# Kernel tuning notes

Measured on AMD Instinct MI355X. Metric: run time of the kernel, lower is better.

The kernel has to match this reference:

```python
import jax, jax.numpy as jnp
import numpy as np

N = 100000   # nodes
E = 1600000  # edges
D = 128      # in_channels
H = 128      # hidden_dim
L = 3        # num_layers
LH = 128     # lstm_hidden
OUT = 16     # output_dim
G = 128      # graphs in batch
EPS = 1e-5   # BatchNorm eps


def setup_inputs() -> dict:
    key = jax.random.key(0)
    ks = jax.random.split(key, 14)
    x = jax.random.normal(ks[0], (N, D), jnp.float32)
    src = jax.random.randint(ks[1], (E,), 0, N)
    dst = jax.random.randint(ks[2], (E,), 0, N)
    edge_index = jnp.stack([src, dst])
    batch = jnp.sort(jax.random.randint(ks[3], (N,), 0, G))
    Ws = jax.random.normal(ks[4], (L, D, H), jnp.float32) / np.float32(np.sqrt(D))
    bs = jax.random.normal(ks[5], (L, H), jnp.float32) * 0.02
    gammas = 1.0 + 0.1 * jax.random.normal(ks[6], (L, H), jnp.float32)
    betas = 0.1 * jax.random.normal(ks[7], (L, H), jnp.float32)
    rms = 0.1 * jax.random.normal(ks[8], (L, H), jnp.float32)
    rvs = jax.random.uniform(ks[9], (L, H), jnp.float32, 0.5, 1.5)
    W_ih = jax.random.normal(ks[10], (4 * LH, H), jnp.float32) / np.float32(np.sqrt(H))
    W_hh = jax.random.normal(ks[11], (4 * LH, LH), jnp.float32) / np.float32(np.sqrt(LH))
    b_ih = jnp.zeros((4 * LH,), jnp.float32)
    b_hh = jnp.zeros((4 * LH,), jnp.float32)
    W_fc = jax.random.normal(ks[12], (OUT, LH), jnp.float32) / np.float32(np.sqrt(LH))
    b_fc = 0.02 * jax.random.normal(ks[13], (OUT,), jnp.float32)
    return dict(x=x, edge_index=edge_index, batch=batch, Ws=Ws, bs=bs,
                gammas=gammas, betas=betas, rms=rms, rvs=rvs,
                W_ih=W_ih, W_hh=W_hh, b_ih=b_ih, b_hh=b_hh, W_fc=W_fc, b_fc=b_fc)


def reference(x, edge_index, batch, Ws, bs, gammas, betas, rms, rvs,
              W_ih, W_hh, b_ih, b_hh, W_fc, b_fc):
    # GCNConv: add self-loops, symmetric deg^-1/2 normalization
    src, dst = edge_index[0], edge_index[1]
    loop = jnp.arange(N)
    s = jnp.concatenate([src, loop])
    d = jnp.concatenate([dst, loop])
    deg = jax.ops.segment_sum(jnp.ones((E + N,), x.dtype), d, num_segments=N)
    dinv = jax.lax.rsqrt(jnp.maximum(deg, 1.0))  # deg >= 1 due to self-loops
    norm = (dinv[s] * dinv[d])[:, None]          # [E+N, 1]
    h = x
    for l in range(L):
        h = h @ Ws[l]                                                  # [N, H]
        agg = jax.ops.segment_sum(h[s] * norm, d, num_segments=N) + bs[l]
        # BatchNorm (eval: running stats) -> dropout (eval: identity) -> ReLU
        y = (agg - rms[l]) * (gammas[l] * jax.lax.rsqrt(rvs[l] + EPS)) + betas[l]
        h = jax.nn.relu(y)
    # global_mean_pool
    sums = jax.ops.segment_sum(h, batch, num_segments=G)               # [G, H]
    cnt = jax.ops.segment_sum(jnp.ones((N,), h.dtype), batch, num_segments=G)
    pooled = sums / jnp.maximum(cnt, 1.0)[:, None]
    # single-timestep LSTM, h0 = c0 = 0 -> forget gate contributes nothing
    gates = pooled @ W_ih.T + b_ih + b_hh                              # [G, 4*LH]
    i, f, g, o = jnp.split(gates, 4, axis=-1)
    c = jax.nn.sigmoid(i) * jnp.tanh(g)
    hn = jax.nn.sigmoid(o) * jnp.tanh(c)
    return hn @ W_fc.T + b_fc                                          # [G, OUT]
```

## Files before the change

### kernel.cpp

```cpp
#include <hip/hip_runtime.h>
#include <math.h>

constexpr int   NN  = 100000;
constexpr int   EE  = 1600000;
constexpr int   HH  = 128;
constexpr int   GG  = 128;
constexpr float EPSV = 1e-5f;
constexpr int   NSB = 256;
constexpr int   SUBW = (NN + NSB - 1) / NSB;
constexpr int   CAP2 = 8192;
constexpr int   GEMM_BLOCKS = (NN + 127) / 128;
constexpr int   EDATA_BLOCKS = (EE + 255) / 256;
constexpr int   WHALF = 64 * 136;
constexpr int   WLAYER = 2 * 2 * WHALF;

typedef __attribute__((ext_vector_type(8))) short  short8;
typedef __attribute__((ext_vector_type(4))) float  f32x4;
typedef __attribute__((ext_vector_type(2))) float  v2f;

__device__ __forceinline__ unsigned short f2bf(float f) {
    union { float f; unsigned u; } v; v.f = f;
    unsigned r = v.u + 0x7FFF + ((v.u >> 16) & 1);
    return (unsigned short)(r >> 16);
}
__device__ __forceinline__ float bf2f(unsigned short b) {
    union { unsigned u; float f; } v; v.u = ((unsigned)b) << 16;
    return v.f;
}

constexpr size_t A256(size_t x) { return (x + 255) & ~(size_t)255; }
constexpr size_t OFF_TL  = 0;
constexpr size_t OFF_DNV = A256(OFF_TL  + 256 * 4);
constexpr size_t OFF_RP  = A256(OFF_DNV + (size_t)NN * 4);
constexpr size_t OFF_SRC = A256(OFF_RP  + (size_t)(NN + 1) * 4);
constexpr size_t OFF_B2  = A256(OFF_SRC + (size_t)EE * 4);
constexpr size_t OFF_ED  = A256(OFF_B2  + (size_t)NSB * CAP2 * 4);
constexpr size_t OFF_WS  = A256(OFF_ED  + (size_t)EE * 8);
constexpr size_t OFF_HW  = A256(OFF_WS  + (size_t)2 * WLAYER * 2);
constexpr size_t OFF_H0  = A256(OFF_HW  + (size_t)NN * HH * 2);
constexpr size_t OFF_PL  = A256(OFF_H0  + (size_t)NN * HH * 2);

template<bool FP32A>
__device__ __forceinline__ void gemm_body(const void* __restrict__ Ap,
                                          const float* __restrict__ W,
                                          const unsigned short* __restrict__ Wsp,
                                          unsigned short* __restrict__ C,
                                          int nrows, int rb) {
    __shared__ unsigned short smem[2 * WHALF];
    unsigned short* WtH = smem;
    unsigned short* WtL = smem + WHALF;
    int t = threadIdx.x;
    int row0 = rb * 128;
    int wv = t >> 6, lane = t & 63, m = lane & 15, q = lane >> 4;
    long rowA = row0 + wv * 32 + m;
    long rowB = rowA + 16;

    short8 a[2][4];
#pragma unroll
    for (int kc = 0; kc < 4; ++kc) {
        int ko = kc * 32 + q * 8;
        if (FP32A) {
            const float* Af = (const float*)Ap;
            float4 f0 = {0,0,0,0}, f1 = {0,0,0,0}, g0 = {0,0,0,0}, g1 = {0,0,0,0};
            if (rowA < nrows) {
                f0 = *(const float4*)(Af + rowA * 128 + ko);
                f1 = *(const float4*)(Af + rowA * 128 + ko + 4);
            }
            if (rowB < nrows) {
                g0 = *(const float4*)(Af + rowB * 128 + ko);
                g1 = *(const float4*)(Af + rowB * 128 + ko + 4);
            }
            union { short8 s; unsigned short u[8]; } ua, ub;
            ua.u[0] = f2bf(f0.x); ua.u[1] = f2bf(f0.y); ua.u[2] = f2bf(f0.z); ua.u[3] = f2bf(f0.w);
            ua.u[4] = f2bf(f1.x); ua.u[5] = f2bf(f1.y); ua.u[6] = f2bf(f1.z); ua.u[7] = f2bf(f1.w);
            ub.u[0] = f2bf(g0.x); ub.u[1] = f2bf(g0.y); ub.u[2] = f2bf(g0.z); ub.u[3] = f2bf(g0.w);
            ub.u[4] = f2bf(g1.x); ub.u[5] = f2bf(g1.y); ub.u[6] = f2bf(g1.z); ub.u[7] = f2bf(g1.w);
            a[0][kc] = ua.s; a[1][kc] = ub.s;
        } else {
            const unsigned short* Ab = (const unsigned short*)Ap;
            short8 z = {};
            a[0][kc] = (rowA < nrows) ? *(const short8*)(Ab + rowA * 128 + ko) : z;
            a[1][kc] = (rowB < nrows) ? *(const short8*)(Ab + rowB * 128 + ko) : z;
        }
    }

    for (int half = 0; half < 2; ++half) {
        int c0 = half * 64;
        __syncthreads();
        if (FP32A) {
            for (int idx = t; idx < 64 * 128; idx += 256) {
                int k = idx >> 6, c = idx & 63;
                float w = W[k * 128 + c0 + c];
                unsigned short hb = f2bf(w);
                WtH[c * 136 + k] = hb;
                WtL[c * 136 + k] = f2bf(w - bf2f(hb));
            }
        } else {
            const uint4* srcw = (const uint4*)(Wsp + (size_t)half * 2 * WHALF);
            uint4* dstw = (uint4*)smem;
            for (int i = t; i < 2176; i += 256) dstw[i] = srcw[i];
        }
        __syncthreads();
        f32x4 acc[2][4] = {};
#pragma unroll
        for (int kc = 0; kc < 4; ++kc) {
            int ko = kc * 32 + q * 8;
#pragma unroll
            for (int ct = 0; ct < 4; ++ct) {
                short8 bh = *(const short8*)(WtH + (ct * 16 + m) * 136 + ko);
                short8 bl = *(const short8*)(WtL + (ct * 16 + m) * 136 + ko);
                acc[0][ct] = __builtin_amdgcn_mfma_f32_16x16x32_bf16(a[0][kc], bh, acc[0][ct], 0, 0, 0);
                acc[0][ct] = __builtin_amdgcn_mfma_f32_16x16x32_bf16(a[0][kc], bl, acc[0][ct], 0, 0, 0);
                acc[1][ct] = __builtin_amdgcn_mfma_f32_16x16x32_bf16(a[1][kc], bh, acc[1][ct], 0, 0, 0);
                acc[1][ct] = __builtin_amdgcn_mfma_f32_16x16x32_bf16(a[1][kc], bl, acc[1][ct], 0, 0, 0);
            }
        }
        __syncthreads();
        unsigned short* Cs = smem;
#pragma unroll
        for (int rt = 0; rt < 2; ++rt)
#pragma unroll
            for (int ct = 0; ct < 4; ++ct)
#pragma unroll
                for (int r = 0; r < 4; ++r) {
                    int rl = wv * 32 + rt * 16 + q * 4 + r;
                    Cs[rl * 68 + ct * 16 + m] = f2bf(acc[rt][ct][r]);
                }
        __syncthreads();
        for (int idx = t; idx < 128 * 16; idx += 256) {
            int row = idx >> 4, ch = idx & 15;
            long grow = row0 + row;
            if (grow < nrows)
                *(ushort4*)(C + grow * 128 + c0 + ch * 4) = *(const ushort4*)(Cs + row * 68 + ch * 4);
        }
    }
}

__device__ void binall_body(const int* __restrict__ src, const int* __restrict__ dst,
                            unsigned* __restrict__ bins2, unsigned* __restrict__ tail2,
                            int b) {
    __shared__ unsigned cnt[NSB];
    __shared__ unsigned cur[NSB];
    int t = threadIdx.x;
    cnt[t] = 0;
    __syncthreads();
    const int nvec = EE / 4;
    int csz = (nvec + NSB - 1) / NSB;
    int i0 = b * csz;
    int i1 = i0 + csz; if (i1 > nvec) i1 = nvec;
    const int4* d4 = (const int4*)dst;
    const int4* s4 = (const int4*)src;
    for (int i = i0 + t; i < i1; i += 256) {
        int4 d = d4[i];
        atomicAdd(&cnt[(unsigned)d.x / SUBW], 1u);
        atomicAdd(&cnt[(unsigned)d.y / SUBW], 1u);
        atomicAdd(&cnt[(unsigned)d.z / SUBW], 1u);
        atomicAdd(&cnt[(unsigned)d.w / SUBW], 1u);
    }
    __syncthreads();
    cur[t] = atomicAdd(&tail2[t], cnt[t]);
    __syncthreads();
    for (int i = i0 + t; i < i1; i += 256) {
        int4 d = d4[i];
        int4 s = s4[i];
        int dd[4] = {d.x, d.y, d.z, d.w};
        int ss[4] = {s.x, s.y, s.z, s.w};
#pragma unroll
        for (int c = 0; c < 4; ++c) {
            unsigned gsb = (unsigned)dd[c] / SUBW;
            unsigned p = atomicAdd(&cur[gsb], 1u);
            if (p < (unsigned)CAP2)
                bins2[(size_t)gsb * CAP2 + p] =
                    ((unsigned)(dd[c] - gsb * SUBW) << 17) | (unsigned)ss[c];
        }
    }
}

__global__ __launch_bounds__(256) void k_gemm0_bin(const float* __restrict__ x,
                                                   const float* __restrict__ W,
                                                   unsigned short* __restrict__ C,
                                                   const int* __restrict__ src,
                                                   const int* __restrict__ dst,
                                                   unsigned* __restrict__ bins2,
                                                   unsigned* __restrict__ tail2) {
    if (blockIdx.x < GEMM_BLOCKS)
        gemm_body<true>(x, W, nullptr, C, NN, blockIdx.x);
    else
        binall_body(src, dst, bins2, tail2, blockIdx.x - GEMM_BLOCKS);
}

__global__ __launch_bounds__(256) void k_gemm(const unsigned short* __restrict__ A,
                                              const unsigned short* __restrict__ Wsp,
                                              unsigned short* __restrict__ C) {
    gemm_body<false>(A, nullptr, Wsp, C, NN, blockIdx.x);
}

__global__ __launch_bounds__(256) void k_build(const unsigned* __restrict__ bins2,
                                               const unsigned* __restrict__ tail2,
                                               int* __restrict__ rp,
                                               float* __restrict__ dinv,
                                               int* __restrict__ ssrc,
                                               float* __restrict__ pooled) {
    __shared__ int hist[SUBW];
    __shared__ int sa[512], sd[512];
    __shared__ unsigned ta[256], tb[256];
    int b = blockIdx.x, t = threadIdx.x;

    if (b < 65) {
        int idx = b * 256 + t;
        if (idx < GG * HH + GG) pooled[idx] = 0.f;
    }

    unsigned v = tail2[t];
    ta[t] = v;
    __syncthreads();
    unsigned *sp = ta, *dp = tb;
    for (int off = 1; off < 256; off <<= 1) {
        dp[t] = sp[t] + ((t >= off) ? sp[t - off] : 0u);
        __syncthreads();
        unsigned* tmp = sp; sp = dp; dp = tmp;
    }
    unsigned base = sp[b] - tail2[b];
    unsigned m = tail2[b];
    if (m > (unsigned)CAP2) m = CAP2;

    int lo = b * SUBW;
    int nn = NN - lo; if (nn > SUBW) nn = SUBW;
    for (int i = t; i < nn; i += 256) hist[i] = 0;
    __syncthreads();

    const unsigned* bb = bins2 + (size_t)b * CAP2;
    unsigned nv = m >> 2;
    for (unsigned i = t; i < nv; i += 256) {
        uint4 u = ((const uint4*)bb)[i];
        atomicAdd(&hist[u.x >> 17], 1);
        atomicAdd(&hist[u.y >> 17], 1);
        atomicAdd(&hist[u.z >> 17], 1);
        atomicAdd(&hist[u.w >> 17], 1);
    }
    for (unsigned i = (m & ~3u) + t; i < m; i += 256)
        atomicAdd(&hist[bb[i] >> 17], 1);
    __syncthreads();

    sa[t]       = (t < nn)       ? hist[t]       : 0;
    sa[t + 256] = (t + 256 < nn) ? hist[t + 256] : 0;
    __syncthreads();
    int* s = sa; int* d = sd;
    for (int off = 1; off < 512; off <<= 1) {
        d[t]       = s[t]       + ((t >= off)       ? s[t - off]       : 0);
        d[t + 256] = s[t + 256] + ((t + 256 >= off) ? s[t + 256 - off] : 0);
        __syncthreads();
        int* tmp = s; s = d; d = tmp;
    }

    for (int i = t; i < nn; i += 256) {
        int cur0 = (int)base + (i ? s[i - 1] : 0);
        rp[lo + i]   = cur0;
        dinv[lo + i] = rsqrtf((float)(hist[i] + 1));
    }
    __syncthreads();
    for (int i = t; i < nn; i += 256)
        hist[i] = (int)base + (i ? s[i - 1] : 0);
    if (b == 255 && t == 0) rp[NN] = EE;
    __syncthreads();

    for (unsigned i = t; i < nv; i += 256) {
        uint4 u = ((const uint4*)bb)[i];
        int p;
        p = atomicAdd(&hist[u.x >> 17], 1); ssrc[p] = (int)(u.x & 0x1FFFFu);
        p = atomicAdd(&hist[u.y >> 17], 1); ssrc[p] = (int)(u.y & 0x1FFFFu);
        p = atomicAdd(&hist[u.z >> 17], 1); ssrc[p] = (int)(u.z & 0x1FFFFu);
        p = atomicAdd(&hist[u.w >> 17], 1); ssrc[p] = (int)(u.w & 0x1FFFFu);
    }
    for (unsigned i = (m & ~3u) + t; i < m; i += 256) {
        unsigned u = bb[i];
        int p = atomicAdd(&hist[u >> 17], 1);
        ssrc[p] = (int)(u & 0x1FFFFu);
    }
}

__global__ void k_edata(const int* __restrict__ ssrc, const float* __restrict__ dinv,
                        uint2* __restrict__ edata, const float* __restrict__ Ws,
                        unsigned short* __restrict__ wsp) {
    int b = blockIdx.x;
    if (b < EDATA_BLOCKS) {
        int i = b * 256 + threadIdx.x;
        if (i < EE) {
            int s = ssrc[i];
            edata[i] = make_uint2((unsigned)s, __float_as_uint(dinv[s]));
        }
    } else {
        int t = threadIdx.x;
        if (t < 128) {
            int e = (b - EDATA_BLOCKS) * 128 + t;
            int l = e >> 14;
            int r = e & 16383;
            int k = r >> 7;
            int c = r & 127;
            int half = c >> 6, cl = c & 63;
            float w = Ws[(size_t)(l + 1) * 16384 + k * 128 + c];
            unsigned short hb = f2bf(w);
            unsigned short lb = f2bf(w - bf2f(hb));
            size_t base = (size_t)l * WLAYER + (size_t)half * 2 * WHALF;
            wsp[base + cl * 136 + k]         = hb;
            wsp[base + WHALF + cl * 136 + k] = lb;
        }
    }
}

__global__ __launch_bounds__(256) void k_agg(const unsigned short* __restrict__ hw,
                                             const int* __restrict__ rp,
                                             const uint2* __restrict__ edata,
                                             const float* __restrict__ dinv,
                                             const float* __restrict__ bsl,
                                             const float* __restrict__ gamma,
                                             const float* __restrict__ beta,
                                             const float* __restrict__ rm,
                                             const float* __restrict__ rv,
                                             unsigned short* __restrict__ out) {
    int lane = threadIdx.x & 63;
    int c2   = lane * 2;
    int n = blockIdx.x * 4 + (threadIdx.x >> 6);
    if (n >= NN) return;
    int beg = rp[n], end = rp[n + 1];

    v2f acc0 = {0.f, 0.f}, acc1 = {0.f, 0.f};

    for (int chunk = beg; chunk < end; chunk += 64) {
        int l = chunk + lane;
        uint2 ed = (l < end) ? edata[l] : make_uint2((unsigned)n, 0u);
        int   e  = (int)ed.x;
        float dv = __uint_as_float(ed.y);
        int cnt = end - chunk;
        if (cnt > 64) cnt = 64;
        for (int jb = 0; jb < cnt; jb += 8) {
#pragma unroll
            for (int j = 0; j < 8; ++j) {
                int s    = __builtin_amdgcn_readlane(e, jb + j);
                float ds = __int_as_float(
                               __builtin_amdgcn_readlane(__float_as_int(dv), jb + j));
                unsigned u = *(const unsigned*)(hw + (size_t)s * HH + c2);
                v2f vv;
                vv.x = __int_as_float((int)(u << 16));
                vv.y = __int_as_float((int)(u & 0xffff0000u));
                v2f d2 = {ds, ds};
                if (j & 1) acc1 += d2 * vv;
                else       acc0 += d2 * vv;
            }
        }
    }
    v2f a = acc0 + acc1;

    float di = dinv[n];
    {
        unsigned u = *(const unsigned*)(hw + (size_t)n * HH + c2);
        v2f vv;
        vv.x = __int_as_float((int)(u << 16));
        vv.y = __int_as_float((int)(u & 0xffff0000u));
        v2f d2 = {di, di};
        a += d2 * vv;
    }
    a.x *= di;
    a.y *= di;

    float g0 = gamma[c2],   g1 = gamma[c2 + 1];
    float r0 = rv[c2],      r1 = rv[c2 + 1];
    float s0 = g0 * rsqrtf(r0 + EPSV);
    float s1 = g1 * rsqrtf(r1 + EPSV);
    float b0 = fmaf(bsl[c2]     - rm[c2],     s0, beta[c2]);
    float b1 = fmaf(bsl[c2 + 1] - rm[c2 + 1], s1, beta[c2 + 1]);
    float y0 = fmaxf(fmaf(a.x, s0, b0), 0.f);
    float y1 = fmaxf(fmaf(a.y, s1, b1), 0.f);
    ushort2 o;
    o.x = f2bf(y0);
    o.y = f2bf(y1);
    *(ushort2*)(out + (size_t)n * HH + c2) = o;
}

__global__ __launch_bounds__(128) void k_pool(const unsigned short* __restrict__ h,
                                              const int* __restrict__ batch,
                                              float* __restrict__ pooled,
                                              float* __restrict__ cnt) {
    int t = threadIdx.x;
    const int chunk = (NN + 1023) / 1024;
    int n0 = blockIdx.x * chunk;
    if (n0 >= NN) return;
    int n1 = n0 + chunk;
    if (n1 > NN) n1 = NN;
    int cur = batch[n0];
    float acc = 0.f;
    int k = 0;
    for (int n = n0; n < n1; ++n) {
        int b = batch[n];
        if (b != cur) {
            atomicAdd(&pooled[(size_t)cur * 128 + t], acc);
            if (t == 0) atomicAdd(&cnt[cur], (float)k);
            acc = 0.f; k = 0; cur = b;
        }
        acc += bf2f(h[(size_t)n * 128 + t]);
        ++k;
    }
    atomicAdd(&pooled[(size_t)cur * 128 + t], acc);
    if (t == 0) atomicAdd(&cnt[cur], (float)k);
}

__global__ __launch_bounds__(128) void k_head(const float* __restrict__ pooled,
                                              const float* __restrict__ cnt,
                                              const float* __restrict__ W_ih,
                                              const float* __restrict__ b_ih,
                                              const float* __restrict__ b_hh,
                                              const float* __restrict__ W_fc,
                                              const float* __restrict__ b_fc,
                                              float* __restrict__ out) {
    __shared__ float pm[128];
    __shared__ float gate[512];
    __shared__ float hn[128];
    int g = blockIdx.x, t = threadIdx.x;
    float cdiv = fmaxf(cnt[g], 1.0f);
    pm[t] = pooled[(size_t)g * 128 + t] / cdiv;
    __syncthreads();
    for (int j = t; j < 512; j += 128) {
        float acc = b_ih[j] + b_hh[j];
        const float* w = W_ih + (size_t)j * 128;
#pragma unroll 8
        for (int k = 0; k < 128; ++k) acc = fmaf(pm[k], w[k], acc);
        gate[j] = acc;
    }
    __syncthreads();
    {
        float gi = gate[t], gg = gate[256 + t], go = gate[384 + t];
        float cc = (1.f / (1.f + expf(-gi))) * tanhf(gg);
        hn[t] = (1.f / (1.f + expf(-go))) * tanhf(cc);
    }
    __syncthreads();
    if (t < 16) {
        float acc = b_fc[t];
        const float* w = W_fc + (size_t)t * 128;
#pragma unroll 8
        for (int k = 0; k < 128; ++k) acc = fmaf(hn[k], w[k], acc);
        out[(size_t)g * 16 + t] = acc;
    }
}

extern "C" void kernel_launch(void* const* d_in, const int* in_sizes, int n_in,
                              void* d_out, int out_size, void* d_ws, size_t ws_size,
                              hipStream_t stream) {
    const float* x      = (const float*)d_in[0];
    const int*   ei     = (const int*)d_in[1];
    const int*   src    = ei;
    const int*   dst    = ei + EE;
    const int*   batch  = (const int*)d_in[2];
    const float* Ws     = (const float*)d_in[3];
    const float* bs     = (const float*)d_in[4];
    const float* gammas = (const float*)d_in[5];
    const float* betas  = (const float*)d_in[6];
    const float* rms    = (const float*)d_in[7];
    const float* rvs    = (const float*)d_in[8];
    const float* W_ih   = (const float*)d_in[9];
    const float* b_ih   = (const float*)d_in[11];
    const float* b_hh   = (const float*)d_in[12];
    const float* W_fc   = (const float*)d_in[13];
    const float* b_fc   = (const float*)d_in[14];
    float* out = (float*)d_out;

    char* w = (char*)d_ws;
    unsigned*       tail2  = (unsigned*)(w + OFF_TL);
    float*          dinv   = (float*)(w + OFF_DNV);
    int*            rp     = (int*)(w + OFF_RP);
    int*            ssrc   = (int*)(w + OFF_SRC);
    unsigned*       bins2  = (unsigned*)(w + OFF_B2);
    uint2*          edata  = (uint2*)(w + OFF_ED);
    unsigned short* wsp    = (unsigned short*)(w + OFF_WS);
    unsigned short* hwb    = (unsigned short*)(w + OFF_HW);
    unsigned short* h0     = (unsigned short*)(w + OFF_H0);
    float*          pooled = (float*)(w + OFF_PL);
    float*          cntb   = pooled + (size_t)GG * HH;

    hipMemsetAsync(tail2, 0, 256 * 4, stream);

    k_gemm0_bin<<<GEMM_BLOCKS + NSB, 256, 0, stream>>>(x, Ws, hwb, src, dst, bins2, tail2);
    k_build<<<NSB, 256, 0, stream>>>(bins2, tail2, rp, dinv, ssrc, pooled);
    k_edata<<<EDATA_BLOCKS + 256, 256, 0, stream>>>(ssrc, dinv, edata, Ws, wsp);

    for (int l = 0; l < 3; ++l) {
        if (l > 0)
            k_gemm<<<GEMM_BLOCKS, 256, 0, stream>>>(h0, wsp + (size_t)(l - 1) * WLAYER, hwb);
        k_agg<<<(NN + 3) / 4, 256, 0, stream>>>(hwb, rp, edata, dinv,
                                                bs + l * 128, gammas + l * 128, betas + l * 128,
                                                rms + l * 128, rvs + l * 128, h0);
    }
    k_pool<<<1024, 128, 0, stream>>>(h0, batch, pooled, cntb);
    k_head<<<GG, 128, 0, stream>>>(pooled, cntb, W_ih, b_ih, b_hh, W_fc, b_fc, out);
}
```

Before: 435.9 us.

## Fuse edge-data build into first aggregation and weight split into build kernel

Removes the separate k_edata kernel. The first-layer aggregation now reads sorted sources and dinv directly and writes the packed edge data that later layers reuse. The weight bf16 hi/lo split moves into extra blocks of k_build. Pooling now uses twice as many blocks, each covering a smaller chunk. This saves one launch and a full pass over the edge arrays, at the cost of a dependent dinv gather and extra stores inside layer-0 aggregation.

```diff
diff --git a/kernel.cpp b/kernel.cpp
--- a/kernel.cpp
+++ b/kernel.cpp
@@ -10,7 +10,6 @@
 constexpr int   SUBW = (NN + NSB - 1) / NSB;
 constexpr int   CAP2 = 8192;
 constexpr int   GEMM_BLOCKS = (NN + 127) / 128;
-constexpr int   EDATA_BLOCKS = (EE + 255) / 256;
 constexpr int   WHALF = 64 * 136;
 constexpr int   WLAYER = 2 * 2 * WHALF;
 
@@ -200,11 +199,30 @@
                                                int* __restrict__ rp,
                                                float* __restrict__ dinv,
                                                int* __restrict__ ssrc,
-                                               float* __restrict__ pooled) {
+                                               float* __restrict__ pooled,
+                                               const float* __restrict__ Ws,
+                                               unsigned short* __restrict__ wsp) {
+    int b = blockIdx.x, t = threadIdx.x;
+
+    if (b >= NSB) {
+        int e = (b - NSB) * 256 + t;
+        int l = e >> 14;
+        int r = e & 16383;
+        int k = r >> 7;
+        int c = r & 127;
+        int half = c >> 6, cl = c & 63;
+        float w = Ws[(size_t)(l + 1) * 16384 + k * 128 + c];
+        unsigned short hb = f2bf(w);
+        unsigned short lb = f2bf(w - bf2f(hb));
+        size_t base = (size_t)l * WLAYER + (size_t)half * 2 * WHALF;
+        wsp[base + cl * 136 + k]         = hb;
+        wsp[base + WHALF + cl * 136 + k] = lb;
+        return;
+    }
+
     __shared__ int hist[SUBW];
     __shared__ int sa[512], sd[512];
     __shared__ unsigned ta[256], tb[256];
-    int b = blockIdx.x, t = threadIdx.x;
 
     if (b < 65) {
         int idx = b * 256 + t;
@@ -279,38 +297,11 @@
     }
 }
 
-__global__ void k_edata(const int* __restrict__ ssrc, const float* __restrict__ dinv,
-                        uint2* __restrict__ edata, const float* __restrict__ Ws,
-                        unsigned short* __restrict__ wsp) {
-    int b = blockIdx.x;
-    if (b < EDATA_BLOCKS) {
-        int i = b * 256 + threadIdx.x;
-        if (i < EE) {
-            int s = ssrc[i];
-            edata[i] = make_uint2((unsigned)s, __float_as_uint(dinv[s]));
-        }
-    } else {
-        int t = threadIdx.x;
-        if (t < 128) {
-            int e = (b - EDATA_BLOCKS) * 128 + t;
-            int l = e >> 14;
-            int r = e & 16383;
-            int k = r >> 7;
-            int c = r & 127;
-            int half = c >> 6, cl = c & 63;
-            float w = Ws[(size_t)(l + 1) * 16384 + k * 128 + c];
-            unsigned short hb = f2bf(w);
-            unsigned short lb = f2bf(w - bf2f(hb));
-            size_t base = (size_t)l * WLAYER + (size_t)half * 2 * WHALF;
-            wsp[base + cl * 136 + k]         = hb;
-            wsp[base + WHALF + cl * 136 + k] = lb;
-        }
-    }
-}
-
+template<bool WRITE_ED>
 __global__ __launch_bounds__(256) void k_agg(const unsigned short* __restrict__ hw,
                                              const int* __restrict__ rp,
-                                             const uint2* __restrict__ edata,
+                                             const int* __restrict__ ssrc,
+                                             uint2* __restrict__ edata,
                                              const float* __restrict__ dinv,
                                              const float* __restrict__ bsl,
                                              const float* __restrict__ gamma,
@@ -328,9 +319,18 @@
 
     for (int chunk = beg; chunk < end; chunk += 64) {
         int l = chunk + lane;
-        uint2 ed = (l < end) ? edata[l] : make_uint2((unsigned)n, 0u);
-        int   e  = (int)ed.x;
-        float dv = __uint_as_float(ed.y);
+        int   e;
+        float dv;
+        if (WRITE_ED) {
+            bool valid = (l < end);
+            e  = valid ? ssrc[l] : n;
+            dv = valid ? dinv[e] : 0.f;
+            if (valid) edata[l] = make_uint2((unsigned)e, __float_as_uint(dv));
+        } else {
+            uint2 ed = (l < end) ? ((const uint2*)edata)[l] : make_uint2((unsigned)n, 0u);
+            e  = (int)ed.x;
+            dv = __uint_as_float(ed.y);
+        }
         int cnt = end - chunk;
         if (cnt > 64) cnt = 64;
         for (int jb = 0; jb < cnt; jb += 8) {
@@ -382,7 +382,7 @@
                                               float* __restrict__ pooled,
                                               float* __restrict__ cnt) {
     int t = threadIdx.x;
-    const int chunk = (NN + 1023) / 1024;
+    const int chunk = (NN + 2047) / 2048;
     int n0 = blockIdx.x * chunk;
     if (n0 >= NN) return;
     int n1 = n0 + chunk;
@@ -479,16 +479,20 @@
     hipMemsetAsync(tail2, 0, 256 * 4, stream);
 
     k_gemm0_bin<<<GEMM_BLOCKS + NSB, 256, 0, stream>>>(x, Ws, hwb, src, dst, bins2, tail2);
-    k_build<<<NSB, 256, 0, stream>>>(bins2, tail2, rp, dinv, ssrc, pooled);
-    k_edata<<<EDATA_BLOCKS + 256, 256, 0, stream>>>(ssrc, dinv, edata, Ws, wsp);
+    k_build<<<NSB + 128, 256, 0, stream>>>(bins2, tail2, rp, dinv, ssrc, pooled, Ws, wsp);
 
     for (int l = 0; l < 3; ++l) {
         if (l > 0)
             k_gemm<<<GEMM_BLOCKS, 256, 0, stream>>>(h0, wsp + (size_t)(l - 1) * WLAYER, hwb);
-        k_agg<<<(NN + 3) / 4, 256, 0, stream>>>(hwb, rp, edata, dinv,
-                                                bs + l * 128, gammas + l * 128, betas + l * 128,
-                                                rms + l * 128, rvs + l * 128, h0);
-    }
-    k_pool<<<1024, 128, 0, stream>>>(h0, batch, pooled, cntb);
+        if (l == 0)
+            k_agg<true><<<(NN + 3) / 4, 256, 0, stream>>>(hwb, rp, ssrc, edata, dinv,
+                                                          bs, gammas, betas, rms, rvs, h0);
+        else
+            k_agg<false><<<(NN + 3) / 4, 256, 0, stream>>>(hwb, rp, ssrc, edata, dinv,
+                                                           bs + l * 128, gammas + l * 128,
+                                                           betas + l * 128, rms + l * 128,
+                                                           rvs + l * 128, h0);
+    }
+    k_pool<<<2048, 128, 0, stream>>>(h0, batch, pooled, cntb);
     k_head<<<GG, 128, 0, stream>>>(pooled, cntb, W_ih, b_ih, b_hh, W_fc, b_fc, out);
 }
```

New measurement: 417.2 us. 4.3% less time.
